# Kernel optimization log

Hardware: AMD Instinct MI355X
Metric: run time of the kernel (lower is better)

The kernel has to match this reference:

```python
import jax, jax.numpy as jnp
import numpy as np

N_NODES = 50000


def _spmm(edge_index, edge_vals, dense):
    """Sparse [N,N] @ dense [N,D] via gather + segment-sum.
    edge_index[0] = row (dst), edge_index[1] = col (src)."""
    dst, src = edge_index[0], edge_index[1]
    msgs = edge_vals[:, None] * dense[src]  # [E, D]
    return jax.ops.segment_sum(msgs, dst, num_segments=N_NODES)


def setup_inputs() -> dict:
    key = jax.random.key(0)
    ks = jax.random.split(key, 8)
    N, D_IN, D_OUT, E = N_NODES, 128, 128, 800000
    x = jax.random.normal(ks[0], (N, D_IN), dtype=jnp.float32)
    # glorot init for weights
    scale = jnp.sqrt(6.0 / (D_IN + D_OUT)).astype(jnp.float32)
    W0 = jax.random.uniform(ks[1], (D_IN, D_OUT), jnp.float32, -scale, scale)
    W1 = jax.random.uniform(ks[2], (D_IN, D_OUT), jnp.float32, -scale, scale)
    bias = jnp.zeros((D_OUT,), dtype=jnp.float32)
    edge_vals0 = jax.random.uniform(ks[3], (E,), dtype=jnp.float32)
    edge_vals1 = jax.random.uniform(ks[4], (E,), dtype=jnp.float32)
    edge_index0 = jax.random.randint(ks[5], (2, E), 0, N, dtype=jnp.int32)
    edge_index1 = jax.random.randint(ks[6], (2, E), 0, N, dtype=jnp.int32)
    return {"x": x, "W0": W0, "W1": W1, "bias": bias,
            "edge_vals0": edge_vals0, "edge_vals1": edge_vals1,
            "edge_index0": edge_index0, "edge_index1": edge_index1}


def reference(x, W0, W1, bias, edge_vals0, edge_vals1, edge_index0, edge_index1):
    # dropout with rate 0 == identity (self.dropout unset in source snippet)
    pre0 = x @ W0  # [N, D_out]
    pre1 = x @ W1
    out = _spmm(edge_index0, edge_vals0, pre0) + _spmm(edge_index1, edge_vals1, pre1)
    out = out + bias
    return jax.nn.relu(out)
```

## Files before the change

kernel.cpp:

```cpp
#include <hip/hip_runtime.h>
#include <hip/hip_bf16.h>


#define BROWS 32
#define NBUCK 1563
#define NB2 2048
#define BCAP 704
#define ACAP (2 * BCAP)
#define FT6 4096
#define PREROWS 65536

typedef __attribute__((ext_vector_type(8))) short bf16x8;
typedef __attribute__((ext_vector_type(4))) float f32x4;

__device__ inline unsigned short f2bf(float f) {
    union { float f; unsigned u; } v; v.f = f;
    unsigned r = v.u + 0x7fff + ((v.u >> 16) & 1);
    return (unsigned short)(r >> 16);
}

__global__ __launch_bounds__(256) void prep_kernel(
    const float* __restrict__ W0, const float* __restrict__ W1,
    unsigned short* __restrict__ wt0, unsigned short* __restrict__ wt1,
    int* __restrict__ cur, int ncur)
{
    const int bid = blockIdx.x;
    const int tid = threadIdx.x;
    if (bid >= 8) {
        for (int i = tid; i < ncur; i += 256) cur[i] = 0;
        return;
    }
    const int which = bid >> 2;
    const int k0 = (bid & 3) * 32;
    const float* __restrict__ W = which ? W1 : W0;
    unsigned short* __restrict__ wt = which ? wt1 : wt0;
    for (int i = tid; i < 32 * 128; i += 256) {
        int k = k0 + (i >> 7), n = i & 127;
        wt[n * 128 + k] = f2bf(W[k * 128 + n]);
    }
}

struct FillSM {
    int2 srt[FT6];
    alignas(16) int lcnt[NB2];
    alignas(16) int lcur[NB2];
    unsigned short skey[FT6];
    int gpos[NBUCK];
    int glim[NBUCK];
    int wsum[8];
    int total;
};
struct GemmSM {
    unsigned short sA[16][136];
    short ctile[8][16][40];
};
union MidSM { FillSM f; GemmSM g; };

__global__ __launch_bounds__(512) void mid_kernel(
    const float* __restrict__ x,
    const unsigned short* __restrict__ wt0,
    const unsigned short* __restrict__ wt1,
    unsigned short* __restrict__ pre,
    const int* __restrict__ ei0, const int* __restrict__ ei1,
    const float* __restrict__ ev0, const float* __restrict__ ev1,
    int* __restrict__ cur, int2* __restrict__ recs,
    int E, int N, int nfill)
{
    __shared__ MidSM sm;
    const int tid = threadIdx.x;
    const int bx = blockIdx.x;

    if (bx < nfill) {
        FillSM& F = sm.f;
        const int a = bx & 1;
        const int e0 = (bx >> 1) * FT6;
        const int* __restrict__ ei = a ? ei1 : ei0;
        const float* __restrict__ ev = a ? ev1 : ev0;

        ((int4*)F.lcnt)[tid] = make_int4(0, 0, 0, 0);
        __syncthreads();

        const int eb = e0 + tid * 8;
        int dd[8], ss[8]; float vv[8];
        if (e0 + FT6 <= E) {
            int4 d0 = *(const int4*)(ei + eb);
            int4 d1 = *(const int4*)(ei + eb + 4);
            int4 s0 = *(const int4*)(ei + E + eb);
            int4 s1 = *(const int4*)(ei + E + eb + 4);
            float4 v0 = *(const float4*)(ev + eb);
            float4 v1 = *(const float4*)(ev + eb + 4);
            dd[0] = d0.x; dd[1] = d0.y; dd[2] = d0.z; dd[3] = d0.w;
            dd[4] = d1.x; dd[5] = d1.y; dd[6] = d1.z; dd[7] = d1.w;
            ss[0] = s0.x; ss[1] = s0.y; ss[2] = s0.z; ss[3] = s0.w;
            ss[4] = s1.x; ss[5] = s1.y; ss[6] = s1.z; ss[7] = s1.w;
            vv[0] = v0.x; vv[1] = v0.y; vv[2] = v0.z; vv[3] = v0.w;
            vv[4] = v1.x; vv[5] = v1.y; vv[6] = v1.z; vv[7] = v1.w;
        } else {
#pragma unroll
            for (int j = 0; j < 8; ++j) {
                int e = eb + j;
                if (e < E) { dd[j] = ei[e]; ss[j] = ei[E + e]; vv[j] = ev[e]; }
            }
        }
        int key8[8]; int2 rec[8];
#pragma unroll
        for (int j = 0; j < 8; ++j) {
            if (eb + j < E) {
                key8[j] = dd[j] >> 5;
                rec[j] = make_int2(((dd[j] & 31) << 17) | (a << 16) | ss[j],
                                   __float_as_int(vv[j]));
                atomicAdd(&F.lcnt[key8[j]], 1);
            } else key8[j] = -1;
        }
        __syncthreads();

        const int lane = tid & 63;
        const int wv = tid >> 6;
        int4 c4 = ((const int4*)F.lcnt)[tid];
        int cc[4] = { c4.x, c4.y, c4.z, c4.w };
        int tsum = cc[0] + cc[1] + cc[2] + cc[3];
        int p = tsum;
#pragma unroll
        for (int o = 1; o < 64; o <<= 1) {
            int t = __shfl_up(p, o);
            if (lane >= o) p += t;
        }
        if (lane == 63) F.wsum[wv] = p;
        __syncthreads();
        int wbase = 0;
#pragma unroll
        for (int w2 = 0; w2 < 7; ++w2) wbase += (w2 < wv) ? F.wsum[w2] : 0;
        if (tid == 511) F.total = wbase + p;
        int off = wbase + p - tsum;
        const int k0 = 4 * tid;
#pragma unroll
        for (int h = 0; h < 4; ++h) {
            F.lcur[k0 + h] = off;
            if (k0 + h < NBUCK && cc[h] > 0) {
                int bin = (k0 + h) * 2 + a;
                int g = atomicAdd(&cur[bin], cc[h]);
                int lim = BCAP - g; if (lim < 0) lim = 0;
                F.gpos[k0 + h] = bin * BCAP + g;
                F.glim[k0 + h] = lim;
            }
            off += cc[h];
        }
        __syncthreads();

#pragma unroll
        for (int j = 0; j < 8; ++j) {
            if (key8[j] >= 0) {
                int pp = atomicAdd(&F.lcur[key8[j]], 1);
                F.srt[pp] = rec[j];
                F.skey[pp] = (unsigned short)key8[j];
            }
        }
        __syncthreads();

        const int total = F.total;
        for (int i = tid; i < total; i += 512) {
            int k = F.skey[i];
            int st = k ? F.lcur[k - 1] : 0;
            int r = i - st;
            if (r < F.glim[k]) recs[F.gpos[k] + r] = F.srt[i];
        }
    } else {
        GemmSM& G = sm.g;
        const int m0 = (bx - nfill) * 16;

        {
            int r = tid >> 5;
            int c4i = (tid & 31) << 2;
            float4 v = *(const float4*)&x[(m0 + r) * 128 + c4i];
            ushort4 s;
            s.x = f2bf(v.x); s.y = f2bf(v.y); s.z = f2bf(v.z); s.w = f2bf(v.w);
            *(ushort4*)&G.sA[r][c4i] = s;
        }
        __syncthreads();

        const int w = tid >> 6;
        const int lane = tid & 63;
        const int adj = w >> 2;
        const int wq = w & 3;
        const unsigned short* __restrict__ wt = adj ? wt1 : wt0;
        unsigned short* __restrict__ po = pre + (size_t)adj * PREROWS * 128;
        const int l15 = lane & 15;
        const int quad = lane >> 4;
        const int nA = wq * 32 + l15;

        f32x4 c0 = {0.f, 0.f, 0.f, 0.f};
        f32x4 c1 = {0.f, 0.f, 0.f, 0.f};
#pragma unroll
        for (int k0 = 0; k0 < 128; k0 += 32) {
            union { bf16x8 v; ushort4 h[2]; } au;
            au.h[0] = *(const ushort4*)&G.sA[l15][k0 + quad * 8];
            au.h[1] = *(const ushort4*)&G.sA[l15][k0 + quad * 8 + 4];
            bf16x8 b0 = *(const bf16x8*)&wt[nA * 128 + k0 + quad * 8];
            bf16x8 b1 = *(const bf16x8*)&wt[(nA + 16) * 128 + k0 + quad * 8];
            c0 = __builtin_amdgcn_mfma_f32_16x16x32_bf16(au.v, b0, c0, 0, 0, 0);
            c1 = __builtin_amdgcn_mfma_f32_16x16x32_bf16(au.v, b1, c1, 0, 0, 0);
        }

#pragma unroll
        for (int i = 0; i < 4; ++i) {
            G.ctile[w][quad * 4 + i][l15]      = (short)f2bf(c0[i]);
            G.ctile[w][quad * 4 + i][16 + l15] = (short)f2bf(c1[i]);
        }
        const int rr = lane >> 2, cg = (lane & 3) * 8;
        ushort4 s0 = *(ushort4*)&G.ctile[w][rr][cg];
        ushort4 s1 = *(ushort4*)&G.ctile[w][rr][cg + 4];
        int row = m0 + rr;
        *(ushort4*)&po[row * 128 + wq * 32 + cg] = s0;
        *(ushort4*)&po[row * 128 + wq * 32 + cg + 4] = s1;
    }
}

__global__ __launch_bounds__(256, 6) void aggregate9_kernel(
    const int* __restrict__ cur, const int2* __restrict__ recs,
    const unsigned short* __restrict__ pre,
    const float* __restrict__ bias,
    float* __restrict__ out, int N)
{
    __shared__ int2 srec[ACAP];
    __shared__ int2 srt[ACAP];
    __shared__ int lcnt[32];
    __shared__ int lstart[32];
    __shared__ int lcur[32];

    const int b = blockIdx.x;
    const int tid = threadIdx.x;

    int n0 = cur[2 * b];     if (n0 > BCAP) n0 = BCAP;
    int n1 = cur[2 * b + 1]; if (n1 > BCAP) n1 = BCAP;
    const int total = n0 + n1;
    const int base0 = (2 * b) * BCAP, base1 = (2 * b + 1) * BCAP;

    if (tid < 32) lcnt[tid] = 0;
    __syncthreads();

    for (int i = tid; i < total; i += 256) {
        int2 r = (i < n0) ? recs[base0 + i] : recs[base1 + i - n0];
        srec[i] = r;
        atomicAdd(&lcnt[(r.x >> 17) & 31], 1);
    }
    __syncthreads();

    if (tid < 32) {
        int cme = lcnt[tid];
        int p = cme;
#pragma unroll
        for (int o = 1; o < 32; o <<= 1) {
            int t = __shfl_up(p, o);
            if (tid >= o) p += t;
        }
        lstart[tid] = p - cme;
        lcur[tid] = p - cme;
    }
    __syncthreads();

    for (int i = tid; i < total; i += 256) {
        int2 r = srec[i];
        srt[atomicAdd(&lcur[(r.x >> 17) & 31], 1)] = r;
    }
    __syncthreads();

    const int wv = tid >> 6;
    const int lane = tid & 63;
    const float2 bi = *(const float2*)&bias[lane * 2];

#define GA(r) (*(const unsigned*)&pre[((r).x & 0x1ffff) * 128 + 2 * lane])
#define ACC(r, u) { float v = __int_as_float((r).y);                    \
        acc.x = fmaf(v, __uint_as_float((u) << 16), acc.x);             \
        acc.y = fmaf(v, __uint_as_float((u) & 0xffff0000u), acc.y); }

    for (int t = 0; t < 8; ++t) {
        const int rl = wv * 8 + t;
        const int s = lstart[rl];
        const int e = s + lcnt[rl];
        float2 acc = make_float2(0.f, 0.f);
        int j = s;
        for (; j + 8 <= e; j += 8) {
            int2 r0 = srt[j], r1 = srt[j + 1], r2 = srt[j + 2], r3 = srt[j + 3];
            int2 r4 = srt[j + 4], r5 = srt[j + 5], r6 = srt[j + 6], r7 = srt[j + 7];
            unsigned u0 = GA(r0), u1 = GA(r1), u2 = GA(r2), u3 = GA(r3);
            unsigned u4 = GA(r4), u5 = GA(r5), u6 = GA(r6), u7 = GA(r7);
            ACC(r0, u0); ACC(r1, u1); ACC(r2, u2); ACC(r3, u3);
            ACC(r4, u4); ACC(r5, u5); ACC(r6, u6); ACC(r7, u7);
        }
        for (; j + 4 <= e; j += 4) {
            int2 r0 = srt[j], r1 = srt[j + 1], r2 = srt[j + 2], r3 = srt[j + 3];
            unsigned u0 = GA(r0), u1 = GA(r1), u2 = GA(r2), u3 = GA(r3);
            ACC(r0, u0); ACC(r1, u1); ACC(r2, u2); ACC(r3, u3);
        }
        for (; j < e; ++j) {
            int2 r0 = srt[j];
            unsigned u0 = GA(r0);
            ACC(r0, u0);
        }
        int row = b * BROWS + rl;
        if (row < N) {
            float2 o;
            o.x = fmaxf(acc.x + bi.x, 0.f);
            o.y = fmaxf(acc.y + bi.y, 0.f);
            *(float2*)&out[row * 128 + 2 * lane] = o;
        }
    }
#undef GA
#undef ACC
}

extern "C" void kernel_launch(void* const* d_in, const int* in_sizes, int n_in,
                              void* d_out, int out_size, void* d_ws, size_t ws_size,
                              hipStream_t stream) {
    const float* x    = (const float*)d_in[0];
    const float* W0   = (const float*)d_in[1];
    const float* W1   = (const float*)d_in[2];
    const float* bias = (const float*)d_in[3];
    const float* ev0  = (const float*)d_in[4];
    const float* ev1  = (const float*)d_in[5];
    const int*   ei0  = (const int*)d_in[6];
    const int*   ei1  = (const int*)d_in[7];
    float* out = (float*)d_out;

    const int N = in_sizes[0] / 128;
    const int E = in_sizes[4];
    const int NBINS2 = NBUCK * 2;

    char* w = (char*)d_ws;
    unsigned short* pre = (unsigned short*)w;   w += (size_t)2 * PREROWS * 128 * 2;
    unsigned short* wt0 = (unsigned short*)w;   w += (size_t)128 * 128 * 2;
    unsigned short* wt1 = (unsigned short*)w;   w += (size_t)128 * 128 * 2;
    int* cur = (int*)w;                         w += (size_t)NBINS2 * 4;
    int2* recs = (int2*)w;                      w += (size_t)NBINS2 * BCAP * 8;

    prep_kernel<<<9, 256, 0, stream>>>(W0, W1, wt0, wt1, cur, NBINS2);

    const int nfill = 2 * ((E + FT6 - 1) / FT6);
    const int ngemm = N / 16;
    mid_kernel<<<nfill + ngemm, 512, 0, stream>>>(
        x, wt0, wt1, pre, ei0, ei1, ev0, ev1, cur, recs, E, N, nfill);

    aggregate9_kernel<<<NBUCK, 256, 0, stream>>>(cur, recs, pre, bias, out, N);
}
```

Baseline: 220.3 us.

## Split fused fill/GEMM kernel and drop staging buffer in aggregate

The combined mid kernel, which branched between edge bucketing and the bf16 MFMA GEMM, is split back into two separate launches. Each launch now uses only its own shared-memory footprint, so the small GEMM blocks no longer reserve the large fill union. The aggregate kernel drops its srec staging array and reads the records from global memory a second time, which cuts its LDS use and raises the occupancy hint from 6 to 8 blocks. The cost is one extra kernel launch, no overlap between fill and GEMM, and a second global read of the records.

```diff
diff --git a/kernel.cpp b/kernel.cpp
--- a/kernel.cpp
+++ b/kernel.cpp
@@ -40,188 +40,180 @@
     }
 }
 
-struct FillSM {
-    int2 srt[FT6];
-    alignas(16) int lcnt[NB2];
-    alignas(16) int lcur[NB2];
-    unsigned short skey[FT6];
-    int gpos[NBUCK];
-    int glim[NBUCK];
-    int wsum[8];
-    int total;
-};
-struct GemmSM {
-    unsigned short sA[16][136];
-    short ctile[8][16][40];
-};
-union MidSM { FillSM f; GemmSM g; };
-
-__global__ __launch_bounds__(512) void mid_kernel(
+__global__ __launch_bounds__(512) void gemm_fused_kernel(
     const float* __restrict__ x,
     const unsigned short* __restrict__ wt0,
     const unsigned short* __restrict__ wt1,
     unsigned short* __restrict__ pre,
+    int N)
+{
+    __shared__ unsigned short sA[16][136];
+    __shared__ short ctile[8][16][40];
+
+    const int tid = threadIdx.x;
+    const int m0 = blockIdx.x * 16;
+
+    {
+        int r = tid >> 5;
+        int c4 = (tid & 31) << 2;
+        float4 v = *(const float4*)&x[(m0 + r) * 128 + c4];
+        ushort4 s;
+        s.x = f2bf(v.x); s.y = f2bf(v.y); s.z = f2bf(v.z); s.w = f2bf(v.w);
+        *(ushort4*)&sA[r][c4] = s;
+    }
+    __syncthreads();
+
+    const int w = tid >> 6;
+    const int lane = tid & 63;
+    const int adj = w >> 2;
+    const int wq = w & 3;
+    const unsigned short* __restrict__ wt = adj ? wt1 : wt0;
+    unsigned short* __restrict__ po = pre + (size_t)adj * PREROWS * 128;
+    const int l15 = lane & 15;
+    const int quad = lane >> 4;
+    const int nA = wq * 32 + l15;
+
+    f32x4 c0 = {0.f, 0.f, 0.f, 0.f};
+    f32x4 c1 = {0.f, 0.f, 0.f, 0.f};
+#pragma unroll
+    for (int k0 = 0; k0 < 128; k0 += 32) {
+        union { bf16x8 v; ushort4 h[2]; } au;
+        au.h[0] = *(const ushort4*)&sA[l15][k0 + quad * 8];
+        au.h[1] = *(const ushort4*)&sA[l15][k0 + quad * 8 + 4];
+        bf16x8 b0 = *(const bf16x8*)&wt[nA * 128 + k0 + quad * 8];
+        bf16x8 b1 = *(const bf16x8*)&wt[(nA + 16) * 128 + k0 + quad * 8];
+        c0 = __builtin_amdgcn_mfma_f32_16x16x32_bf16(au.v, b0, c0, 0, 0, 0);
+        c1 = __builtin_amdgcn_mfma_f32_16x16x32_bf16(au.v, b1, c1, 0, 0, 0);
+    }
+
+#pragma unroll
+    for (int i = 0; i < 4; ++i) {
+        ctile[w][quad * 4 + i][l15]      = (short)f2bf(c0[i]);
+        ctile[w][quad * 4 + i][16 + l15] = (short)f2bf(c1[i]);
+    }
+    const int rr = lane >> 2, cg = (lane & 3) * 8;
+    ushort4 s0 = *(ushort4*)&ctile[w][rr][cg];
+    ushort4 s1 = *(ushort4*)&ctile[w][rr][cg + 4];
+    int row = m0 + rr;
+    *(ushort4*)&po[row * 128 + wq * 32 + cg] = s0;
+    *(ushort4*)&po[row * 128 + wq * 32 + cg + 4] = s1;
+}
+
+__global__ __launch_bounds__(512) void fill6_kernel(
     const int* __restrict__ ei0, const int* __restrict__ ei1,
     const float* __restrict__ ev0, const float* __restrict__ ev1,
-    int* __restrict__ cur, int2* __restrict__ recs,
-    int E, int N, int nfill)
+    int* __restrict__ cur, int2* __restrict__ recs, int E)
 {
-    __shared__ MidSM sm;
+    __shared__ int2 srt[FT6];
+    __shared__ alignas(16) int lcnt[NB2];
+    __shared__ alignas(16) int lcur[NB2];
+    __shared__ unsigned short skey[FT6];
+    __shared__ int gpos[NBUCK];
+    __shared__ int glim[NBUCK];
+    __shared__ int wsum[8];
+    __shared__ int stotal;
+
     const int tid = threadIdx.x;
-    const int bx = blockIdx.x;
-
-    if (bx < nfill) {
-        FillSM& F = sm.f;
-        const int a = bx & 1;
-        const int e0 = (bx >> 1) * FT6;
-        const int* __restrict__ ei = a ? ei1 : ei0;
-        const float* __restrict__ ev = a ? ev1 : ev0;
-
-        ((int4*)F.lcnt)[tid] = make_int4(0, 0, 0, 0);
-        __syncthreads();
-
-        const int eb = e0 + tid * 8;
-        int dd[8], ss[8]; float vv[8];
-        if (e0 + FT6 <= E) {
-            int4 d0 = *(const int4*)(ei + eb);
-            int4 d1 = *(const int4*)(ei + eb + 4);
-            int4 s0 = *(const int4*)(ei + E + eb);
-            int4 s1 = *(const int4*)(ei + E + eb + 4);
-            float4 v0 = *(const float4*)(ev + eb);
-            float4 v1 = *(const float4*)(ev + eb + 4);
-            dd[0] = d0.x; dd[1] = d0.y; dd[2] = d0.z; dd[3] = d0.w;
-            dd[4] = d1.x; dd[5] = d1.y; dd[6] = d1.z; dd[7] = d1.w;
-            ss[0] = s0.x; ss[1] = s0.y; ss[2] = s0.z; ss[3] = s0.w;
-            ss[4] = s1.x; ss[5] = s1.y; ss[6] = s1.z; ss[7] = s1.w;
-            vv[0] = v0.x; vv[1] = v0.y; vv[2] = v0.z; vv[3] = v0.w;
-            vv[4] = v1.x; vv[5] = v1.y; vv[6] = v1.z; vv[7] = v1.w;
-        } else {
-#pragma unroll
-            for (int j = 0; j < 8; ++j) {
-                int e = eb + j;
-                if (e < E) { dd[j] = ei[e]; ss[j] = ei[E + e]; vv[j] = ev[e]; }
-            }
-        }
-        int key8[8]; int2 rec[8];
+    const int a = blockIdx.y;
+    const int e0 = blockIdx.x * FT6;
+    const int* __restrict__ ei = a ? ei1 : ei0;
+    const float* __restrict__ ev = a ? ev1 : ev0;
+
+    ((int4*)lcnt)[tid] = make_int4(0, 0, 0, 0);
+    __syncthreads();
+
+    const int eb = e0 + tid * 8;
+    int dd[8], ss[8]; float vv[8];
+    if (e0 + FT6 <= E) {
+        int4 d0 = *(const int4*)(ei + eb);
+        int4 d1 = *(const int4*)(ei + eb + 4);
+        int4 s0 = *(const int4*)(ei + E + eb);
+        int4 s1 = *(const int4*)(ei + E + eb + 4);
+        float4 v0 = *(const float4*)(ev + eb);
+        float4 v1 = *(const float4*)(ev + eb + 4);
+        dd[0] = d0.x; dd[1] = d0.y; dd[2] = d0.z; dd[3] = d0.w;
+        dd[4] = d1.x; dd[5] = d1.y; dd[6] = d1.z; dd[7] = d1.w;
+        ss[0] = s0.x; ss[1] = s0.y; ss[2] = s0.z; ss[3] = s0.w;
+        ss[4] = s1.x; ss[5] = s1.y; ss[6] = s1.z; ss[7] = s1.w;
+        vv[0] = v0.x; vv[1] = v0.y; vv[2] = v0.z; vv[3] = v0.w;
+        vv[4] = v1.x; vv[5] = v1.y; vv[6] = v1.z; vv[7] = v1.w;
+    } else {
 #pragma unroll
         for (int j = 0; j < 8; ++j) {
-            if (eb + j < E) {
-                key8[j] = dd[j] >> 5;
-                rec[j] = make_int2(((dd[j] & 31) << 17) | (a << 16) | ss[j],
-                                   __float_as_int(vv[j]));
-                atomicAdd(&F.lcnt[key8[j]], 1);
-            } else key8[j] = -1;
-        }
-        __syncthreads();
-
-        const int lane = tid & 63;
-        const int wv = tid >> 6;
-        int4 c4 = ((const int4*)F.lcnt)[tid];
-        int cc[4] = { c4.x, c4.y, c4.z, c4.w };
-        int tsum = cc[0] + cc[1] + cc[2] + cc[3];
-        int p = tsum;
-#pragma unroll
-        for (int o = 1; o < 64; o <<= 1) {
-            int t = __shfl_up(p, o);
-            if (lane >= o) p += t;
-        }
-        if (lane == 63) F.wsum[wv] = p;
-        __syncthreads();
-        int wbase = 0;
-#pragma unroll
-        for (int w2 = 0; w2 < 7; ++w2) wbase += (w2 < wv) ? F.wsum[w2] : 0;
-        if (tid == 511) F.total = wbase + p;
-        int off = wbase + p - tsum;
-        const int k0 = 4 * tid;
-#pragma unroll
-        for (int h = 0; h < 4; ++h) {
-            F.lcur[k0 + h] = off;
-            if (k0 + h < NBUCK && cc[h] > 0) {
-                int bin = (k0 + h) * 2 + a;
-                int g = atomicAdd(&cur[bin], cc[h]);
-                int lim = BCAP - g; if (lim < 0) lim = 0;
-                F.gpos[k0 + h] = bin * BCAP + g;
-                F.glim[k0 + h] = lim;
-            }
-            off += cc[h];
-        }
-        __syncthreads();
-
-#pragma unroll
-        for (int j = 0; j < 8; ++j) {
-            if (key8[j] >= 0) {
-                int pp = atomicAdd(&F.lcur[key8[j]], 1);
-                F.srt[pp] = rec[j];
-                F.skey[pp] = (unsigned short)key8[j];
-            }
-        }
-        __syncthreads();
-
-        const int total = F.total;
-        for (int i = tid; i < total; i += 512) {
-            int k = F.skey[i];
-            int st = k ? F.lcur[k - 1] : 0;
-            int r = i - st;
-            if (r < F.glim[k]) recs[F.gpos[k] + r] = F.srt[i];
-        }
-    } else {
-        GemmSM& G = sm.g;
-        const int m0 = (bx - nfill) * 16;
-
-        {
-            int r = tid >> 5;
-            int c4i = (tid & 31) << 2;
-            float4 v = *(const float4*)&x[(m0 + r) * 128 + c4i];
-            ushort4 s;
-            s.x = f2bf(v.x); s.y = f2bf(v.y); s.z = f2bf(v.z); s.w = f2bf(v.w);
-            *(ushort4*)&G.sA[r][c4i] = s;
-        }
-        __syncthreads();
-
-        const int w = tid >> 6;
-        const int lane = tid & 63;
-        const int adj = w >> 2;
-        const int wq = w & 3;
-        const unsigned short* __restrict__ wt = adj ? wt1 : wt0;
-        unsigned short* __restrict__ po = pre + (size_t)adj * PREROWS * 128;
-        const int l15 = lane & 15;
-        const int quad = lane >> 4;
-        const int nA = wq * 32 + l15;
-
-        f32x4 c0 = {0.f, 0.f, 0.f, 0.f};
-        f32x4 c1 = {0.f, 0.f, 0.f, 0.f};
-#pragma unroll
-        for (int k0 = 0; k0 < 128; k0 += 32) {
-            union { bf16x8 v; ushort4 h[2]; } au;
-            au.h[0] = *(const ushort4*)&G.sA[l15][k0 + quad * 8];
-            au.h[1] = *(const ushort4*)&G.sA[l15][k0 + quad * 8 + 4];
-            bf16x8 b0 = *(const bf16x8*)&wt[nA * 128 + k0 + quad * 8];
-            bf16x8 b1 = *(const bf16x8*)&wt[(nA + 16) * 128 + k0 + quad * 8];
-            c0 = __builtin_amdgcn_mfma_f32_16x16x32_bf16(au.v, b0, c0, 0, 0, 0);
-            c1 = __builtin_amdgcn_mfma_f32_16x16x32_bf16(au.v, b1, c1, 0, 0, 0);
-        }
-
-#pragma unroll
-        for (int i = 0; i < 4; ++i) {
-            G.ctile[w][quad * 4 + i][l15]      = (short)f2bf(c0[i]);
-            G.ctile[w][quad * 4 + i][16 + l15] = (short)f2bf(c1[i]);
-        }
-        const int rr = lane >> 2, cg = (lane & 3) * 8;
-        ushort4 s0 = *(ushort4*)&G.ctile[w][rr][cg];
-        ushort4 s1 = *(ushort4*)&G.ctile[w][rr][cg + 4];
-        int row = m0 + rr;
-        *(ushort4*)&po[row * 128 + wq * 32 + cg] = s0;
-        *(ushort4*)&po[row * 128 + wq * 32 + cg + 4] = s1;
-    }
-}
-
-__global__ __launch_bounds__(256, 6) void aggregate9_kernel(
+            int e = eb + j;
+            if (e < E) { dd[j] = ei[e]; ss[j] = ei[E + e]; vv[j] = ev[e]; }
+        }
+    }
+    int key8[8]; int2 rec[8];
+#pragma unroll
+    for (int j = 0; j < 8; ++j) {
+        if (eb + j < E) {
+            key8[j] = dd[j] >> 5;
+            rec[j] = make_int2(((dd[j] & 31) << 17) | (a << 16) | ss[j],
+                               __float_as_int(vv[j]));
+            atomicAdd(&lcnt[key8[j]], 1);
+        } else key8[j] = -1;
+    }
+    __syncthreads();
+
+    const int lane = tid & 63;
+    const int wv = tid >> 6;
+    int4 c4 = ((const int4*)lcnt)[tid];
+    int cc[4] = { c4.x, c4.y, c4.z, c4.w };
+    int tsum = cc[0] + cc[1] + cc[2] + cc[3];
+    int p = tsum;
+#pragma unroll
+    for (int o = 1; o < 64; o <<= 1) {
+        int t = __shfl_up(p, o);
+        if (lane >= o) p += t;
+    }
+    if (lane == 63) wsum[wv] = p;
+    __syncthreads();
+    int wbase = 0;
+#pragma unroll
+    for (int w2 = 0; w2 < 7; ++w2) wbase += (w2 < wv) ? wsum[w2] : 0;
+    if (tid == 511) stotal = wbase + p;
+    int off = wbase + p - tsum;
+    const int k0 = 4 * tid;
+#pragma unroll
+    for (int h = 0; h < 4; ++h) {
+        lcur[k0 + h] = off;
+        if (k0 + h < NBUCK && cc[h] > 0) {
+            int bin = (k0 + h) * 2 + a;
+            int g = atomicAdd(&cur[bin], cc[h]);
+            int lim = BCAP - g; if (lim < 0) lim = 0;
+            gpos[k0 + h] = bin * BCAP + g;
+            glim[k0 + h] = lim;
+        }
+        off += cc[h];
+    }
+    __syncthreads();
+
+#pragma unroll
+    for (int j = 0; j < 8; ++j) {
+        if (key8[j] >= 0) {
+            int pp = atomicAdd(&lcur[key8[j]], 1);
+            srt[pp] = rec[j];
+            skey[pp] = (unsigned short)key8[j];
+        }
+    }
+    __syncthreads();
+
+    const int total = stotal;
+    for (int i = tid; i < total; i += 512) {
+        int k = skey[i];
+        int st = k ? lcur[k - 1] : 0;
+        int r = i - st;
+        if (r < glim[k]) recs[gpos[k] + r] = srt[i];
+    }
+}
+
+__global__ __launch_bounds__(256, 8) void aggregate10_kernel(
     const int* __restrict__ cur, const int2* __restrict__ recs,
     const unsigned short* __restrict__ pre,
     const float* __restrict__ bias,
     float* __restrict__ out, int N)
 {
-    __shared__ int2 srec[ACAP];
     __shared__ int2 srt[ACAP];
     __shared__ int lcnt[32];
     __shared__ int lstart[32];
@@ -240,7 +232,6 @@
 
     for (int i = tid; i < total; i += 256) {
         int2 r = (i < n0) ? recs[base0 + i] : recs[base1 + i - n0];
-        srec[i] = r;
         atomicAdd(&lcnt[(r.x >> 17) & 31], 1);
     }
     __syncthreads();
@@ -259,7 +250,7 @@
     __syncthreads();
 
     for (int i = tid; i < total; i += 256) {
-        int2 r = srec[i];
+        int2 r = (i < n0) ? recs[base0 + i] : recs[base1 + i - n0];
         srt[atomicAdd(&lcur[(r.x >> 17) & 31], 1)] = r;
     }
     __syncthreads();
@@ -335,10 +326,10 @@
 
     prep_kernel<<<9, 256, 0, stream>>>(W0, W1, wt0, wt1, cur, NBINS2);
 
-    const int nfill = 2 * ((E + FT6 - 1) / FT6);
-    const int ngemm = N / 16;
-    mid_kernel<<<nfill + ngemm, 512, 0, stream>>>(
-        x, wt0, wt1, pre, ei0, ei1, ev0, ev1, cur, recs, E, N, nfill);
-
-    aggregate9_kernel<<<NBUCK, 256, 0, stream>>>(cur, recs, pre, bias, out, N);
-}
+    gemm_fused_kernel<<<N / 16, 512, 0, stream>>>(x, wt0, wt1, pre, N);
+
+    dim3 fgrid((E + FT6 - 1) / FT6, 2);
+    fill6_kernel<<<fgrid, 512, 0, stream>>>(ei0, ei1, ev0, ev1, cur, recs, E);
+
+    aggregate10_kernel<<<NBUCK, 256, 0, stream>>>(cur, recs, pre, bias, out, N);
+}
```

Measured after the change: 226.2 us. 2.7% more time.

## Shrink fill tiles with packed 16-bit counters and enlarge GEMM row tiles

Applied to the files above, without the earlier changes.

The fill blocks now handle 2048 edges each instead of 4096 and pack the per-bucket counts and cursors as two 16-bit halves per int. Bucket positions and limits are recomputed from a single atomic result rather than kept in separate shared arrays. This cuts shared memory per block so more blocks can be resident (launch bounds now request 8). GEMM blocks now cover 64 rows with four M-subtiles, which reuses the weight fragments across subtiles and issues fewer, wider 16-byte stores, adding bounds checks on N. The risk is that twice as many fill blocks mean more global atomics on the bucket counters.

```diff
diff --git a/kernel.cpp b/kernel.cpp
--- a/kernel.cpp
+++ b/kernel.cpp
@@ -7,7 +7,7 @@
 #define NB2 2048
 #define BCAP 704
 #define ACAP (2 * BCAP)
-#define FT6 4096
+#define FT7 2048
 #define PREROWS 65536
 
 typedef __attribute__((ext_vector_type(8))) short bf16x8;
@@ -41,22 +41,25 @@
 }
 
 struct FillSM {
-    int2 srt[FT6];
-    alignas(16) int lcnt[NB2];
-    alignas(16) int lcur[NB2];
-    unsigned short skey[FT6];
-    int gpos[NBUCK];
-    int glim[NBUCK];
+    int2 srt[FT7];
+    int lcntp[NB2 / 2];
+    int lcurp[NB2 / 2];
+    unsigned short skey[FT7];
+    int gg[NBUCK];
     int wsum[8];
     int total;
 };
 struct GemmSM {
-    unsigned short sA[16][136];
+    unsigned short sA[64][136];
     short ctile[8][16][40];
 };
 union MidSM { FillSM f; GemmSM g; };
 
-__global__ __launch_bounds__(512) void mid_kernel(
+__device__ inline int pk_get(const int* p, int k) {
+    return (int)(((unsigned)p[k >> 1] >> ((k & 1) * 16)) & 0xffffu);
+}
+
+__global__ __launch_bounds__(512, 8) void mid_kernel(
     const float* __restrict__ x,
     const unsigned short* __restrict__ wt0,
     const unsigned short* __restrict__ wt1,
@@ -69,55 +72,50 @@
     __shared__ MidSM sm;
     const int tid = threadIdx.x;
     const int bx = blockIdx.x;
+    const int lane = tid & 63;
+    const int wv = tid >> 6;
 
     if (bx < nfill) {
         FillSM& F = sm.f;
         const int a = bx & 1;
-        const int e0 = (bx >> 1) * FT6;
+        const int e0 = (bx >> 1) * FT7;
         const int* __restrict__ ei = a ? ei1 : ei0;
         const float* __restrict__ ev = a ? ev1 : ev0;
 
-        ((int4*)F.lcnt)[tid] = make_int4(0, 0, 0, 0);
-        __syncthreads();
-
-        const int eb = e0 + tid * 8;
-        int dd[8], ss[8]; float vv[8];
-        if (e0 + FT6 <= E) {
-            int4 d0 = *(const int4*)(ei + eb);
-            int4 d1 = *(const int4*)(ei + eb + 4);
-            int4 s0 = *(const int4*)(ei + E + eb);
-            int4 s1 = *(const int4*)(ei + E + eb + 4);
-            float4 v0 = *(const float4*)(ev + eb);
-            float4 v1 = *(const float4*)(ev + eb + 4);
-            dd[0] = d0.x; dd[1] = d0.y; dd[2] = d0.z; dd[3] = d0.w;
-            dd[4] = d1.x; dd[5] = d1.y; dd[6] = d1.z; dd[7] = d1.w;
-            ss[0] = s0.x; ss[1] = s0.y; ss[2] = s0.z; ss[3] = s0.w;
-            ss[4] = s1.x; ss[5] = s1.y; ss[6] = s1.z; ss[7] = s1.w;
-            vv[0] = v0.x; vv[1] = v0.y; vv[2] = v0.z; vv[3] = v0.w;
-            vv[4] = v1.x; vv[5] = v1.y; vv[6] = v1.z; vv[7] = v1.w;
+        ((int2*)F.lcntp)[tid] = make_int2(0, 0);
+        __syncthreads();
+
+        const int eb = e0 + tid * 4;
+        int dd[4], ss[4]; float vv[4];
+        if (e0 + FT7 <= E) {
+            int4 d = *(const int4*)(ei + eb);
+            int4 s = *(const int4*)(ei + E + eb);
+            float4 v = *(const float4*)(ev + eb);
+            dd[0] = d.x; dd[1] = d.y; dd[2] = d.z; dd[3] = d.w;
+            ss[0] = s.x; ss[1] = s.y; ss[2] = s.z; ss[3] = s.w;
+            vv[0] = v.x; vv[1] = v.y; vv[2] = v.z; vv[3] = v.w;
         } else {
 #pragma unroll
-            for (int j = 0; j < 8; ++j) {
+            for (int j = 0; j < 4; ++j) {
                 int e = eb + j;
                 if (e < E) { dd[j] = ei[e]; ss[j] = ei[E + e]; vv[j] = ev[e]; }
             }
         }
-        int key8[8]; int2 rec[8];
-#pragma unroll
-        for (int j = 0; j < 8; ++j) {
+        int key4[4]; int2 rec[4];
+#pragma unroll
+        for (int j = 0; j < 4; ++j) {
             if (eb + j < E) {
-                key8[j] = dd[j] >> 5;
+                key4[j] = dd[j] >> 5;
                 rec[j] = make_int2(((dd[j] & 31) << 17) | (a << 16) | ss[j],
                                    __float_as_int(vv[j]));
-                atomicAdd(&F.lcnt[key8[j]], 1);
-            } else key8[j] = -1;
-        }
-        __syncthreads();
-
-        const int lane = tid & 63;
-        const int wv = tid >> 6;
-        int4 c4 = ((const int4*)F.lcnt)[tid];
-        int cc[4] = { c4.x, c4.y, c4.z, c4.w };
+                atomicAdd(&F.lcntp[key4[j] >> 1], 1 << ((key4[j] & 1) * 16));
+            } else key4[j] = -1;
+        }
+        __syncthreads();
+
+        int p0 = F.lcntp[2 * tid], p1 = F.lcntp[2 * tid + 1];
+        int cc[4] = { p0 & 0xffff, (int)((unsigned)p0 >> 16),
+                      p1 & 0xffff, (int)((unsigned)p1 >> 16) };
         int tsum = cc[0] + cc[1] + cc[2] + cc[3];
         int p = tsum;
 #pragma unroll
@@ -133,26 +131,27 @@
         if (tid == 511) F.total = wbase + p;
         int off = wbase + p - tsum;
         const int k0 = 4 * tid;
+        F.lcurp[2 * tid]     = off | ((off + cc[0]) << 16);
+        F.lcurp[2 * tid + 1] = (off + cc[0] + cc[1]) |
+                               ((off + cc[0] + cc[1] + cc[2]) << 16);
 #pragma unroll
         for (int h = 0; h < 4; ++h) {
-            F.lcur[k0 + h] = off;
-            if (k0 + h < NBUCK && cc[h] > 0) {
-                int bin = (k0 + h) * 2 + a;
-                int g = atomicAdd(&cur[bin], cc[h]);
-                int lim = BCAP - g; if (lim < 0) lim = 0;
-                F.gpos[k0 + h] = bin * BCAP + g;
-                F.glim[k0 + h] = lim;
-            }
-            off += cc[h];
-        }
-        __syncthreads();
-
-#pragma unroll
-        for (int j = 0; j < 8; ++j) {
-            if (key8[j] >= 0) {
-                int pp = atomicAdd(&F.lcur[key8[j]], 1);
+            int k = k0 + h;
+            if (k < NBUCK && cc[h] > 0) {
+                int bin = k * 2 + a;
+                F.gg[k] = atomicAdd(&cur[bin], cc[h]);
+            }
+        }
+        __syncthreads();
+
+#pragma unroll
+        for (int j = 0; j < 4; ++j) {
+            if (key4[j] >= 0) {
+                int sh = (key4[j] & 1) * 16;
+                unsigned old = atomicAdd(&F.lcurp[key4[j] >> 1], 1 << sh);
+                int pp = (old >> sh) & 0xffff;
                 F.srt[pp] = rec[j];
-                F.skey[pp] = (unsigned short)key8[j];
+                F.skey[pp] = (unsigned short)key4[j];
             }
         }
         __syncthreads();
@@ -160,58 +159,64 @@
         const int total = F.total;
         for (int i = tid; i < total; i += 512) {
             int k = F.skey[i];
-            int st = k ? F.lcur[k - 1] : 0;
+            int st = k ? pk_get(F.lcurp, k - 1) : 0;
             int r = i - st;
-            if (r < F.glim[k]) recs[F.gpos[k] + r] = F.srt[i];
+            int g = F.gg[k];
+            int lim = BCAP - g; if (lim < 0) lim = 0;
+            if (r < lim) recs[(k * 2 + a) * BCAP + g + r] = F.srt[i];
         }
     } else {
         GemmSM& G = sm.g;
-        const int m0 = (bx - nfill) * 16;
-
-        {
-            int r = tid >> 5;
-            int c4i = (tid & 31) << 2;
-            float4 v = *(const float4*)&x[(m0 + r) * 128 + c4i];
-            ushort4 s;
-            s.x = f2bf(v.x); s.y = f2bf(v.y); s.z = f2bf(v.z); s.w = f2bf(v.w);
-            *(ushort4*)&G.sA[r][c4i] = s;
-        }
-        __syncthreads();
-
-        const int w = tid >> 6;
-        const int lane = tid & 63;
-        const int adj = w >> 2;
-        const int wq = w & 3;
+        const int m0 = (bx - nfill) * 64;
+
+#pragma unroll
+        for (int t = 0; t < 4; ++t) {
+            int idx = t * 512 + tid;
+            int r = idx >> 5;
+            int c4 = (idx & 31) << 2;
+            if (m0 + r < N) {
+                float4 v = *(const float4*)&x[(size_t)(m0 + r) * 128 + c4];
+                ushort4 s;
+                s.x = f2bf(v.x); s.y = f2bf(v.y); s.z = f2bf(v.z); s.w = f2bf(v.w);
+                *(ushort4*)&G.sA[r][c4] = s;
+            }
+        }
+        __syncthreads();
+
+        const int adj = wv >> 2;
+        const int wq = wv & 3;
         const unsigned short* __restrict__ wt = adj ? wt1 : wt0;
         unsigned short* __restrict__ po = pre + (size_t)adj * PREROWS * 128;
         const int l15 = lane & 15;
         const int quad = lane >> 4;
         const int nA = wq * 32 + l15;
-
-        f32x4 c0 = {0.f, 0.f, 0.f, 0.f};
-        f32x4 c1 = {0.f, 0.f, 0.f, 0.f};
-#pragma unroll
-        for (int k0 = 0; k0 < 128; k0 += 32) {
-            union { bf16x8 v; ushort4 h[2]; } au;
-            au.h[0] = *(const ushort4*)&G.sA[l15][k0 + quad * 8];
-            au.h[1] = *(const ushort4*)&G.sA[l15][k0 + quad * 8 + 4];
-            bf16x8 b0 = *(const bf16x8*)&wt[nA * 128 + k0 + quad * 8];
-            bf16x8 b1 = *(const bf16x8*)&wt[(nA + 16) * 128 + k0 + quad * 8];
-            c0 = __builtin_amdgcn_mfma_f32_16x16x32_bf16(au.v, b0, c0, 0, 0, 0);
-            c1 = __builtin_amdgcn_mfma_f32_16x16x32_bf16(au.v, b1, c1, 0, 0, 0);
-        }
-
-#pragma unroll
-        for (int i = 0; i < 4; ++i) {
-            G.ctile[w][quad * 4 + i][l15]      = (short)f2bf(c0[i]);
-            G.ctile[w][quad * 4 + i][16 + l15] = (short)f2bf(c1[i]);
-        }
         const int rr = lane >> 2, cg = (lane & 3) * 8;
-        ushort4 s0 = *(ushort4*)&G.ctile[w][rr][cg];
-        ushort4 s1 = *(ushort4*)&G.ctile[w][rr][cg + 4];
-        int row = m0 + rr;
-        *(ushort4*)&po[row * 128 + wq * 32 + cg] = s0;
-        *(ushort4*)&po[row * 128 + wq * 32 + cg + 4] = s1;
+
+#pragma unroll
+        for (int mt = 0; mt < 4; ++mt) {
+            f32x4 c0 = {0.f, 0.f, 0.f, 0.f};
+            f32x4 c1 = {0.f, 0.f, 0.f, 0.f};
+#pragma unroll
+            for (int kk = 0; kk < 4; ++kk) {
+                union { bf16x8 v; ushort4 h[2]; } au;
+                au.h[0] = *(const ushort4*)&G.sA[mt * 16 + l15][kk * 32 + quad * 8];
+                au.h[1] = *(const ushort4*)&G.sA[mt * 16 + l15][kk * 32 + quad * 8 + 4];
+                bf16x8 b0 = *(const bf16x8*)&wt[nA * 128 + kk * 32 + quad * 8];
+                bf16x8 b1 = *(const bf16x8*)&wt[(nA + 16) * 128 + kk * 32 + quad * 8];
+                c0 = __builtin_amdgcn_mfma_f32_16x16x32_bf16(au.v, b0, c0, 0, 0, 0);
+                c1 = __builtin_amdgcn_mfma_f32_16x16x32_bf16(au.v, b1, c1, 0, 0, 0);
+            }
+#pragma unroll
+            for (int i = 0; i < 4; ++i) {
+                G.ctile[wv][quad * 4 + i][l15]      = (short)f2bf(c0[i]);
+                G.ctile[wv][quad * 4 + i][16 + l15] = (short)f2bf(c1[i]);
+            }
+            int row = m0 + mt * 16 + rr;
+            if (row < N) {
+                int4 sv = *(const int4*)&G.ctile[wv][rr][cg];
+                *(int4*)&po[(size_t)row * 128 + wq * 32 + cg] = sv;
+            }
+        }
     }
 }
 
@@ -335,8 +340,8 @@
 
     prep_kernel<<<9, 256, 0, stream>>>(W0, W1, wt0, wt1, cur, NBINS2);
 
-    const int nfill = 2 * ((E + FT6 - 1) / FT6);
-    const int ngemm = N / 16;
+    const int nfill = 2 * ((E + FT7 - 1) / FT7);
+    const int ngemm = (N + 63) / 64;
     mid_kernel<<<nfill + ngemm, 512, 0, stream>>>(
         x, wt0, wt1, pre, ei0, ei1, ev0, ev1, cur, recs, E, N, nfill);
 
```

Result: slower. 244.2 us (+10.8%).
